# Performance work log

Hardware: AMD Instinct MI355X
Metric: run time of the kernel (lower is better)

Reference implementation:

```python
import jax, jax.numpy as jnp
import numpy as np

D_MODEL = 64
SEQ_LEN = 9
MAX_SL = 50
TIMESTAMP = 56
ACTION_NUM = 300
BATCH = 65536


def setup_inputs() -> dict:
    key = jax.random.key(0)
    ks = jax.random.split(key, 8)
    input_actions = jax.random.randint(ks[0], (BATCH, SEQ_LEN), 0, ACTION_NUM + 1)
    emb_table = jax.random.normal(ks[1], (ACTION_NUM + 1, D_MODEL), jnp.float32) * 0.02
    emb_table = emb_table.at[0].set(0.0)  # padding_idx=0
    M_w = jax.random.normal(ks[2], (MAX_SL, D_MODEL, D_MODEL), jnp.float32) * 0.05
    M_b = jax.random.normal(ks[3], (MAX_SL, D_MODEL), jnp.float32) * 0.05
    W_w = jax.random.normal(ks[4], (TIMESTAMP, D_MODEL, D_MODEL), jnp.float32) * 0.05
    W_b = jax.random.normal(ks[5], (TIMESTAMP, D_MODEL), jnp.float32) * 0.05
    out_w = jax.random.normal(ks[6], (ACTION_NUM, D_MODEL), jnp.float32) * 0.05
    out_b = jax.random.normal(ks[7], (ACTION_NUM,), jnp.float32) * 0.05
    return {"input_actions": input_actions, "emb_table": emb_table,
            "M_w": M_w, "M_b": M_b, "W_w": W_w, "W_b": W_b,
            "out_w": out_w, "out_b": out_b}


def reference(input_actions, emb_table, M_w, M_b, W_w, W_b, out_w, out_b):
    B, S = input_actions.shape
    d = emb_table.shape[1]
    ae = emb_table[input_actions]              # [B, S, d]
    ae_t = jnp.transpose(ae, (1, 0, 2))        # [S, B, d]
    # per-timestep weight selection, matching M[min(i, len(M)-1)] and W[i % timeStamp]
    m_idx = jnp.minimum(jnp.arange(S), M_w.shape[0] - 1)
    w_idx = jnp.arange(S) % W_w.shape[0]
    Mw, Mb = M_w[m_idx], M_b[m_idx]            # [S, d, d], [S, d]
    Ww, Wb = W_w[w_idx], W_b[w_idx]

    def step(hl, xs):
        x, mw, mb, ww, wb = xs
        # torch Linear: y = x @ W.T + b
        hl = jax.nn.sigmoid(x @ mw.T + mb + hl @ ww.T + wb)
        return hl, None

    hl0 = jnp.zeros((B, d), ae.dtype)
    hl, _ = jax.lax.scan(step, hl0, (ae_t, Mw, Mb, Ww, Wb))
    return hl @ out_w.T + out_b               # [B, actionNum]
```

## Files before the change

kernel.cpp:

```cpp
#include <hip/hip_runtime.h>
#include <hip/hip_bf16.h>


#define BATCH   65536
#define SEQ     9
#define DMODEL  64
#define ANUM    300
#define LSTR    72

#define WS_M    0
#define WS_W    36864
#define WS_OW   73728
#define WS_EMB  94208
#define WS_END  113472
#define WS_BSUM_BYTES (WS_END * 2)

typedef __attribute__((ext_vector_type(8))) short  bf16x8;
typedef __attribute__((ext_vector_type(4))) float  f32x4;

__device__ __forceinline__ unsigned short f2b(float f) {
    union { float f; unsigned int u; } x; x.f = f;
    unsigned int r = x.u + 0x7FFFu + ((x.u >> 16) & 1u);
    return (unsigned short)(r >> 16);
}

__device__ __forceinline__ float sigmoid_fast(float v) {
    return __builtin_amdgcn_rcpf(1.f + __expf(-v));
}

#define PP_TOTAL (36864 + 20480 + 19264 + 576)

__global__ void prepack(const float* __restrict__ Mw, const float* __restrict__ Ww,
                        const float* __restrict__ outw, const float* __restrict__ emb,
                        const float* __restrict__ Mb, const float* __restrict__ Wb,
                        unsigned short* __restrict__ wsb, float* __restrict__ bsum)
{
    int t = blockIdx.x * 256 + threadIdx.x;
    if (t < 36864) {
        int j    = t & 7;
        int lane = (t >> 3) & 63;
        int kb   = (t >> 9) & 1;
        int nt   = (t >> 10) & 3;
        int s    = t >> 12;
        int nr   = nt * 16 + (lane & 15);
        int k    = kb * 32 + ((lane >> 4) << 3) + j;
        wsb[WS_M + t] = f2b(Mw[(s * DMODEL + nr) * DMODEL + k]);
        wsb[WS_W + t] = f2b(Ww[(s * DMODEL + nr) * DMODEL + k]);
        return;
    }
    t -= 36864;
    if (t < 20480) {
        int j    = t & 7;
        int lane = (t >> 3) & 63;
        int kb   = (t >> 9) & 1;
        int nt   = (t >> 10) & 3;
        int cc   = t >> 12;
        int col  = cc * 64 + nt * 16 + (lane & 15);
        int k    = kb * 32 + ((lane >> 4) << 3) + j;
        float v  = (col < ANUM) ? outw[col * DMODEL + k] : 0.f;
        wsb[WS_OW + t] = f2b(v);
        return;
    }
    t -= 20480;
    if (t < 19264) { wsb[WS_EMB + t] = f2b(emb[t]); return; }
    t -= 19264;
    if (t < 576)   { bsum[t] = Mb[t] + Wb[t]; }
}

__global__ __launch_bounds__(128, 8)
void carnn_main(const int* __restrict__ acts,
                const unsigned short* __restrict__ wsb,
                const float* __restrict__ bsum,
                const float* __restrict__ outb,
                float* __restrict__ out)
{
    __shared__ unsigned short Hl[2][16 * LSTR];

    const int tid  = threadIdx.x;
    const int lane = tid & 63;
    const int w01  = tid >> 6;
    const int lrow = lane & 15;
    const int quad = lane >> 4;

    const int brow = blockIdx.x * 16 + lrow;

    for (int i = tid; i < 16 * LSTR; i += 128) Hl[0][i] = 0;
    __syncthreads();

    const unsigned short* Mp = wsb + WS_M;
    const unsigned short* Wp = wsb + WS_W;
    const unsigned short* Op = wsb + WS_OW;
    const unsigned short* Eb = wsb + WS_EMB;

    const int hoff = lrow * LSTR + quad * 8;

    #pragma unroll
    for (int s = 0; s < SEQ; ++s) {
        const int rb = s & 1, wb = rb ^ 1;

        bf16x8 ah0 = *(const bf16x8*)&Hl[rb][hoff];
        bf16x8 ah1 = *(const bf16x8*)&Hl[rb][hoff + 32];

        int id = acts[brow * SEQ + s];
        const bf16x8* ex = (const bf16x8*)(Eb + id * DMODEL);
        bf16x8 ax0 = ex[quad];
        bf16x8 ax1 = ex[4 + quad];

        #pragma unroll
        for (int ntl = 0; ntl < 2; ++ntl) {
            const int nt = w01 * 2 + ntl;
            const int fo = (s * 4 + nt) * 1024 + lane * 8;
            bf16x8 bm0 = *(const bf16x8*)&Mp[fo];
            bf16x8 bm1 = *(const bf16x8*)&Mp[fo + 512];
            bf16x8 bw0 = *(const bf16x8*)&Wp[fo];
            bf16x8 bw1 = *(const bf16x8*)&Wp[fo + 512];

            f32x4 acc = {0.f, 0.f, 0.f, 0.f};
            acc = __builtin_amdgcn_mfma_f32_16x16x32_bf16(ax0, bm0, acc, 0, 0, 0);
            acc = __builtin_amdgcn_mfma_f32_16x16x32_bf16(ax1, bm1, acc, 0, 0, 0);
            acc = __builtin_amdgcn_mfma_f32_16x16x32_bf16(ah0, bw0, acc, 0, 0, 0);
            acc = __builtin_amdgcn_mfma_f32_16x16x32_bf16(ah1, bw1, acc, 0, 0, 0);

            const int col  = nt * 16 + lrow;
            const float bias = bsum[s * DMODEL + col];
            const int wr = (quad * 4) * LSTR + col;
            #pragma unroll
            for (int r = 0; r < 4; ++r) {
                float h = sigmoid_fast(acc[r] + bias);
                Hl[wb][wr + r * LSTR] = f2b(h);
            }
        }
        __syncthreads();
    }

    bf16x8 ah0 = *(const bf16x8*)&Hl[1][hoff];
    bf16x8 ah1 = *(const bf16x8*)&Hl[1][hoff + 32];
    const int rowb = blockIdx.x * 16 + quad * 4;

    #pragma unroll
    for (int cc = 0; cc < 5; ++cc) {
        #pragma unroll
        for (int ntl = 0; ntl < 2; ++ntl) {
            const int nt = w01 * 2 + ntl;
            const int fo = (cc * 4 + nt) * 1024 + lane * 8;
            bf16x8 b0 = *(const bf16x8*)&Op[fo];
            bf16x8 b1 = *(const bf16x8*)&Op[fo + 512];
            f32x4 acc = {0.f, 0.f, 0.f, 0.f};
            acc = __builtin_amdgcn_mfma_f32_16x16x32_bf16(ah0, b0, acc, 0, 0, 0);
            acc = __builtin_amdgcn_mfma_f32_16x16x32_bf16(ah1, b1, acc, 0, 0, 0);

            const int col = cc * 64 + nt * 16 + lrow;
            if (col < ANUM) {
                const float bias = outb[col];
                #pragma unroll
                for (int r = 0; r < 4; ++r)
                    out[(rowb + r) * ANUM + col] = acc[r] + bias;
            }
        }
    }
}

extern "C" void kernel_launch(void* const* d_in, const int* in_sizes, int n_in,
                              void* d_out, int out_size, void* d_ws, size_t ws_size,
                              hipStream_t stream) {
    const int*   acts = (const int*)  d_in[0];
    const float* emb  = (const float*)d_in[1];
    const float* Mw   = (const float*)d_in[2];
    const float* Mb   = (const float*)d_in[3];
    const float* Ww   = (const float*)d_in[4];
    const float* Wb   = (const float*)d_in[5];
    const float* outw = (const float*)d_in[6];
    const float* outb = (const float*)d_in[7];
    float* out = (float*)d_out;
    (void)in_sizes; (void)n_in; (void)ws_size; (void)out_size;

    unsigned short* wsb = (unsigned short*)d_ws;
    float* bsum = (float*)((char*)d_ws + WS_BSUM_BYTES);

    prepack<<<(PP_TOTAL + 255) / 256, 256, 0, stream>>>(Mw, Ww, outw, emb, Mb, Wb, wsb, bsum);
    carnn_main<<<BATCH / 16, 128, 0, stream>>>(acts, wsb, bsum, outb, out);
}
```

Measured before the change: 139.4 us.

## Stage per-step weights in LDS with async double-buffering across 128-row blocks

Blocks grow from 16 to 128 rows and 1024 threads, and prepack interleaves M and W per timestep. Each step's weight fragments are copied once into LDS with global_load_lds and double-buffered, so eight teams of waves share them instead of each wave reading them from global or L2. The output projection weights are streamed the same way, adding a barrier per output chunk. This cuts redundant weight traffic but adds synchronization, and the large blocks with extra LDS may lower occupancy and leave only 512 blocks to spread across the GPU.

```diff
diff --git a/kernel.cpp b/kernel.cpp
--- a/kernel.cpp
+++ b/kernel.cpp
@@ -2,14 +2,13 @@
 #include <hip/hip_bf16.h>
 
 
-#define BATCH   65536
 #define SEQ     9
 #define DMODEL  64
 #define ANUM    300
+#define RPB     128
 #define LSTR    72
 
-#define WS_M    0
-#define WS_W    36864
+#define WS_MW   0
 #define WS_OW   73728
 #define WS_EMB  94208
 #define WS_END  113472
@@ -28,7 +27,13 @@
     return __builtin_amdgcn_rcpf(1.f + __expf(-v));
 }
 
-#define PP_TOTAL (36864 + 20480 + 19264 + 576)
+__device__ __forceinline__ void async16(const unsigned short* g, unsigned short* l) {
+    __builtin_amdgcn_global_load_lds(
+        (const __attribute__((address_space(1))) unsigned int*)g,
+        (__attribute__((address_space(3))) unsigned int*)l, 16, 0, 0);
+}
+
+#define PP_TOTAL (73728 + 20480 + 19264 + 576)
 
 __global__ void prepack(const float* __restrict__ Mw, const float* __restrict__ Ww,
                         const float* __restrict__ outw, const float* __restrict__ emb,
@@ -36,19 +41,22 @@
                         unsigned short* __restrict__ wsb, float* __restrict__ bsum)
 {
     int t = blockIdx.x * 256 + threadIdx.x;
-    if (t < 36864) {
-        int j    = t & 7;
-        int lane = (t >> 3) & 63;
-        int kb   = (t >> 9) & 1;
-        int nt   = (t >> 10) & 3;
-        int s    = t >> 12;
+    if (t < 73728) {
+        int s    = t >> 13;
+        int r    = t & 8191;
+        int kind = r >> 12;
+        int f    = r & 4095;
+        int nt   = f >> 10;
+        int kb   = (f >> 9) & 1;
+        int lane = (f >> 3) & 63;
+        int j    = f & 7;
         int nr   = nt * 16 + (lane & 15);
         int k    = kb * 32 + ((lane >> 4) << 3) + j;
-        wsb[WS_M + t] = f2b(Mw[(s * DMODEL + nr) * DMODEL + k]);
-        wsb[WS_W + t] = f2b(Ww[(s * DMODEL + nr) * DMODEL + k]);
+        const float* src = kind ? Ww : Mw;
+        wsb[WS_MW + t] = f2b(src[(s * DMODEL + nr) * DMODEL + k]);
         return;
     }
-    t -= 36864;
+    t -= 73728;
     if (t < 20480) {
         int j    = t & 7;
         int lane = (t >> 3) & 63;
@@ -67,53 +75,62 @@
     if (t < 576)   { bsum[t] = Mb[t] + Wb[t]; }
 }
 
-__global__ __launch_bounds__(128, 8)
+__global__ __launch_bounds__(1024, 8)
 void carnn_main(const int* __restrict__ acts,
                 const unsigned short* __restrict__ wsb,
                 const float* __restrict__ bsum,
                 const float* __restrict__ outb,
                 float* __restrict__ out)
 {
-    __shared__ unsigned short Hl[2][16 * LSTR];
+    __shared__ unsigned short Wf[2][8192];
+    __shared__ unsigned short Hl[2][RPB * LSTR];
 
     const int tid  = threadIdx.x;
     const int lane = tid & 63;
-    const int w01  = tid >> 6;
+    const int wv   = tid >> 6;
+    const int team = wv >> 1;
+    const int half = wv & 1;
     const int lrow = lane & 15;
     const int quad = lane >> 4;
 
-    const int brow = blockIdx.x * 16 + lrow;
-
-    for (int i = tid; i < 16 * LSTR; i += 128) Hl[0][i] = 0;
+    const int brow = blockIdx.x * RPB + team * 16 + lrow;
+    const int hoff = (team * 16 + lrow) * LSTR + quad * 8;
+
+    for (int i = tid; i < RPB * LSTR; i += 1024) Hl[0][i] = 0;
+    async16(wsb + WS_MW + tid * 8, &Wf[0][wv * 512]);
+
+    const unsigned short* Eb = wsb + WS_EMB;
+    int idcur = acts[brow * SEQ];
+
     __syncthreads();
-
-    const unsigned short* Mp = wsb + WS_M;
-    const unsigned short* Wp = wsb + WS_W;
-    const unsigned short* Op = wsb + WS_OW;
-    const unsigned short* Eb = wsb + WS_EMB;
-
-    const int hoff = lrow * LSTR + quad * 8;
 
     #pragma unroll
     for (int s = 0; s < SEQ; ++s) {
         const int rb = s & 1, wb = rb ^ 1;
 
+        const bf16x8* ex = (const bf16x8*)(Eb + idcur * DMODEL);
+        bf16x8 ax0 = ex[quad];
+        bf16x8 ax1 = ex[4 + quad];
+
+        if (s + 1 < SEQ) {
+            idcur = acts[brow * SEQ + s + 1];
+            async16(wsb + WS_MW + (s + 1) * 8192 + tid * 8, &Wf[wb][wv * 512]);
+        } else {
+            if (wv < 8) async16(wsb + WS_OW + tid * 8, &Wf[wb][wv * 512]);
+        }
+
         bf16x8 ah0 = *(const bf16x8*)&Hl[rb][hoff];
         bf16x8 ah1 = *(const bf16x8*)&Hl[rb][hoff + 32];
 
-        int id = acts[brow * SEQ + s];
-        const bf16x8* ex = (const bf16x8*)(Eb + id * DMODEL);
-        bf16x8 ax0 = ex[quad];
-        bf16x8 ax1 = ex[4 + quad];
-
         #pragma unroll
         for (int ntl = 0; ntl < 2; ++ntl) {
-            const int nt = w01 * 2 + ntl;
-            const int fo = (s * 4 + nt) * 1024 + lane * 8;
-            bf16x8 bm0 = *(const bf16x8*)&Mp[fo];
-            bf16x8 bm1 = *(const bf16x8*)&Mp[fo + 512];
-            bf16x8 bw0 = *(const bf16x8*)&Wp[fo];
-            bf16x8 bw1 = *(const bf16x8*)&Wp[fo + 512];
+            const int nt = half * 2 + ntl;
+            const unsigned short* Mf  = &Wf[rb][nt * 1024 + lane * 8];
+            const unsigned short* Wfp = &Wf[rb][4096 + nt * 1024 + lane * 8];
+            bf16x8 bm0 = *(const bf16x8*)Mf;
+            bf16x8 bm1 = *(const bf16x8*)(Mf + 512);
+            bf16x8 bw0 = *(const bf16x8*)Wfp;
+            bf16x8 bw1 = *(const bf16x8*)(Wfp + 512);
 
             f32x4 acc = {0.f, 0.f, 0.f, 0.f};
             acc = __builtin_amdgcn_mfma_f32_16x16x32_bf16(ax0, bm0, acc, 0, 0, 0);
@@ -123,7 +140,7 @@
 
             const int col  = nt * 16 + lrow;
             const float bias = bsum[s * DMODEL + col];
-            const int wr = (quad * 4) * LSTR + col;
+            const int wr = (team * 16 + quad * 4) * LSTR + col;
             #pragma unroll
             for (int r = 0; r < 4; ++r) {
                 float h = sigmoid_fast(acc[r] + bias);
@@ -135,16 +152,21 @@
 
     bf16x8 ah0 = *(const bf16x8*)&Hl[1][hoff];
     bf16x8 ah1 = *(const bf16x8*)&Hl[1][hoff + 32];
-    const int rowb = blockIdx.x * 16 + quad * 4;
+    const int rowb = blockIdx.x * RPB + team * 16 + quad * 4;
 
     #pragma unroll
     for (int cc = 0; cc < 5; ++cc) {
+        const int rbuf = (cc + 1) & 1;
+        const int wbuf = rbuf ^ 1;
+        if (cc + 1 < 5 && wv < 8)
+            async16(wsb + WS_OW + (cc + 1) * 4096 + tid * 8, &Wf[wbuf][wv * 512]);
+
         #pragma unroll
         for (int ntl = 0; ntl < 2; ++ntl) {
-            const int nt = w01 * 2 + ntl;
-            const int fo = (cc * 4 + nt) * 1024 + lane * 8;
-            bf16x8 b0 = *(const bf16x8*)&Op[fo];
-            bf16x8 b1 = *(const bf16x8*)&Op[fo + 512];
+            const int nt = half * 2 + ntl;
+            const unsigned short* Of = &Wf[rbuf][nt * 1024 + lane * 8];
+            bf16x8 b0 = *(const bf16x8*)Of;
+            bf16x8 b1 = *(const bf16x8*)(Of + 512);
             f32x4 acc = {0.f, 0.f, 0.f, 0.f};
             acc = __builtin_amdgcn_mfma_f32_16x16x32_bf16(ah0, b0, acc, 0, 0, 0);
             acc = __builtin_amdgcn_mfma_f32_16x16x32_bf16(ah1, b1, acc, 0, 0, 0);
@@ -157,6 +179,7 @@
                     out[(rowb + r) * ANUM + col] = acc[r] + bias;
             }
         }
+        if (cc + 1 < 5) __syncthreads();
     }
 }
 
@@ -178,5 +201,5 @@
     float* bsum = (float*)((char*)d_ws + WS_BSUM_BYTES);
 
     prepack<<<(PP_TOTAL + 255) / 256, 256, 0, stream>>>(Mw, Ww, outw, emb, Mb, Wb, wsb, bsum);
-    carnn_main<<<BATCH / 16, 128, 0, stream>>>(acts, wsb, bsum, outb, out);
-}
+    carnn_main<<<65536 / RPB, 1024, 0, stream>>>(acts, wsb, bsum, outb, out);
+}
```

Measured after the change: 124.2 us. 1.12x faster.
